# Kernel tuning notes

Measured on AMD Instinct MI355X. Metric: run time of the kernel, lower is better.

The kernel has to match this reference:

```python
import jax, jax.numpy as jnp
import numpy as np

COMMITMENT_COST = 0.25


def setup_inputs() -> dict:
    key = jax.random.key(0)
    k1, k2 = jax.random.split(key)
    ze = jax.random.normal(k1, (16, 256, 32, 32), dtype=jnp.float32)
    codebook = jax.random.normal(k2, (8192, 256), dtype=jnp.float32) * 0.02
    return {"ze": ze, "codebook": codebook}


def reference(ze, codebook):
    # ze: [B, C, H, W] -> [B, H, W, C]
    B, C, H, W = ze.shape
    ze_nhwc = jnp.transpose(ze, (0, 2, 3, 1))
    ze_flat = ze_nhwc.reshape(B * H * W, C)

    # squared L2 distances to every codebook row: [B*H*W, vocab]
    distances = (
        jnp.sum(ze_flat ** 2, axis=1, keepdims=True)
        + jnp.sum(codebook ** 2, axis=1)
        - 2.0 * ze_flat @ codebook.T
    )
    encoding_indices = jnp.argmin(distances, axis=1)  # [B*H*W]
    zq = codebook[encoding_indices].reshape(B, H, W, C)

    sg = jax.lax.stop_gradient
    quantization_loss = jnp.mean((sg(ze_nhwc) - zq) ** 2)
    commitment_loss = jnp.mean((ze_nhwc - sg(zq)) ** 2)
    vq_loss = quantization_loss + COMMITMENT_COST * commitment_loss

    # straight-through estimator (training mode)
    zq = ze_nhwc + sg(zq - ze_nhwc)
    zq = jnp.transpose(zq, (0, 3, 1, 2))  # back to [B, C, H, W]
    return vq_loss, zq, encoding_indices.reshape(B, H * W)
```

## Files before the change

kernel.cpp:

```cpp
#include <hip/hip_runtime.h>
#include <hip/hip_bf16.h>

#define NPIX 16384
#define NVOC 8192
#define CHUNK 32

typedef short short8v __attribute__((ext_vector_type(8)));
typedef float floatx4 __attribute__((ext_vector_type(4)));

#define WS_ZEBF   0u
#define WS_BLIST  0u
#define WS_PART   0u
#define WS_CBBF   8388608u
#define WS_PK     8388608u
#define WS_TAU    8519680u
#define WS_ZEF    12582912u
#define WS_MIN    29360128u
#define WS_BN     37748736u
#define WS_AN     37781504u
#define WS_BCNT   37847040u
#define WS_BMAXU  37847552u
#define WS_QCNT   37847556u
#define WS_QUEUE  37847808u

__device__ __forceinline__ short f2bf(float v) {
  __bf16 h = (__bf16)v;
  return __builtin_bit_cast(short, h);
}

__device__ __forceinline__ float rl(float v, int l) {
  return __uint_as_float(__builtin_amdgcn_readlane(__float_as_uint(v), l));
}

__device__ __forceinline__ unsigned long long packdj(float d, int j) {
  return ((unsigned long long)__float_as_uint(d) << 32) | (unsigned int)j;
}

__device__ __forceinline__ void gll16(const void* g, void* l) {
  __builtin_amdgcn_global_load_lds(
      (const __attribute__((address_space(1))) void*)g,
      (__attribute__((address_space(3))) void*)l, 16, 0, 0);
}

__device__ __forceinline__ float np_pairwise128_sq(const float* x, int stride) {
  float r[8];
#pragma unroll
  for (int j = 0; j < 8; ++j) {
    float v = x[j * stride];
    r[j] = __fmul_rn(v, v);
  }
#pragma unroll
  for (int i = 1; i < 16; ++i) {
#pragma unroll
    for (int j = 0; j < 8; ++j) {
      float v = x[(i * 8 + j) * stride];
      r[j] = __fadd_rn(r[j], __fmul_rn(v, v));
    }
  }
  return __fadd_rn(__fadd_rn(__fadd_rn(r[0], r[1]), __fadd_rn(r[2], r[3])),
                   __fadd_rn(__fadd_rn(r[4], r[5]), __fadd_rn(r[6], r[7])));
}

__global__ __launch_bounds__(256) void k_bnorm(const float* __restrict__ cb,
                                               float* __restrict__ bn,
                                               unsigned* __restrict__ bmaxu) {
  __shared__ float rows[64][257];
  int tid = threadIdx.x;
  int c0 = blockIdx.x * 64;
  for (int r = 0; r < 64; ++r)
    rows[r][tid] = cb[(size_t)(c0 + r) * 256 + tid];
  __syncthreads();
  if (tid < 64) {
    float a = np_pairwise128_sq(&rows[tid][0], 1);
    float b = np_pairwise128_sq(&rows[tid][128], 1);
    float v = __fadd_rn(a, b);
    bn[c0 + tid] = v;
    atomicMax(bmaxu, __float_as_uint(v));
  }
}

__global__ __launch_bounds__(256) void k_cvt_ze(const float* __restrict__ ze,
                                                short* __restrict__ zebff,
                                                float* __restrict__ zef,
                                                float* __restrict__ an) {
  __shared__ float t[64][132];
  int tid = threadIdx.x;
  int p0 = blockIdx.x * 64;
  int b = p0 >> 10, hw0 = p0 & 1023;
  const float* src = ze + (size_t)b * 262144 + hw0;
  float apart = 0.f;
  for (int half = 0; half < 2; ++half) {
    if (half) __syncthreads();
    {
      int hw = tid & 63, cq = tid >> 6;
#pragma unroll
      for (int i = 0; i < 32; ++i) {
        int cl = i * 4 + cq;
        t[hw][cl] = src[(size_t)(half * 128 + cl) * 1024 + hw];
      }
    }
    __syncthreads();
    {
      int r = tid >> 2, cg = tid & 3;
      float* fd = zef + (size_t)(p0 + r) * 256 + half * 128 + cg * 32;
#pragma unroll
      for (int s = 0; s < 8; ++s) {
        float4 v = *reinterpret_cast<const float4*>(&t[r][cg * 32 + s * 4]);
        *reinterpret_cast<float4*>(fd + s * 4) = v;
      }
    }
    {
      int pg_l = tid >> 6, l = tid & 63;
      size_t pg = (size_t)(p0 >> 4) + pg_l;
      int lr = l & 15, lg = l >> 4;
#pragma unroll
      for (int kl = 0; kl < 4; ++kl) {
        int ks = half * 4 + kl;
        short8v v8;
#pragma unroll
        for (int e = 0; e < 8; ++e)
          v8[e] = f2bf(t[pg_l * 16 + lr][kl * 32 + lg * 8 + e]);
        *reinterpret_cast<short8v*>(zebff + (pg * 8 + ks) * 512 + l * 8) = v8;
      }
    }
    if (tid < 64) {
      float a = np_pairwise128_sq(&t[tid][0], 1);
      apart = half ? __fadd_rn(apart, a) : a;
    }
  }
  if (tid < 64) an[p0 + tid] = apart;
}

__global__ __launch_bounds__(256) void k_cvt_cb(const float* __restrict__ cb,
                                                short* __restrict__ cbbft,
                                                unsigned* __restrict__ bmaxu,
                                                int* __restrict__ qcnt) {
  __shared__ short t[64][264];
  int tid = threadIdx.x;
  if (blockIdx.x == 0 && tid == 0) {
    bmaxu[0] = 0u;
    qcnt[0] = 0;
  }
  int j0 = blockIdx.x * 64;
  {
    int col = tid >> 2, q = tid & 3;
    const float* src = cb + (size_t)(j0 + col) * 256 + q * 64;
#pragma unroll
    for (int i = 0; i < 8; ++i) {
      float4 a = *reinterpret_cast<const float4*>(src + i * 8);
      float4 b = *reinterpret_cast<const float4*>(src + i * 8 + 4);
      short8v v;
      v[0] = f2bf(a.x); v[1] = f2bf(a.y); v[2] = f2bf(a.z); v[3] = f2bf(a.w);
      v[4] = f2bf(b.x); v[5] = f2bf(b.y); v[6] = f2bf(b.z); v[7] = f2bf(b.w);
      *reinterpret_cast<short8v*>(&t[col][q * 64 + i * 8]) = v;
    }
  }
  __syncthreads();
  short* dst = cbbft + (size_t)blockIdx.x * 16384;
#pragma unroll
  for (int s = 0; s < 8; ++s) {
    int cid = tid + s * 256;
    int kc = cid >> 6, c2 = cid & 63;
    short8v v = *reinterpret_cast<const short8v*>(&t[c2][kc * 8]);
    *reinterpret_cast<short8v*>(dst + cid * 8) = v;
  }
}

__global__ __launch_bounds__(256, 2) void k_gemm(const short* __restrict__ zebff,
                                                 const short* __restrict__ cbbft,
                                                 const float* __restrict__ bn,
                                                 float* __restrict__ wsmin) {
  __shared__ short lds[32768];
  __shared__ float bnlds[1024];
  int tid = threadIdx.x;
  int lane = tid & 63, w = tid >> 6;
  int g = lane >> 4, r16 = lane & 15;
  int oct = blockIdx.x & 7, chunk = blockIdx.x >> 3;
  int p0 = chunk * 256;
  int ncol0 = oct * 1024;

  short8v pix[4][8];
  {
    const short* base = zebff + ((size_t)(p0 >> 4) + w * 4) * 4096 + lane * 8;
#pragma unroll
    for (int pf = 0; pf < 4; ++pf)
#pragma unroll
      for (int ks = 0; ks < 8; ++ks)
        pix[pf][ks] =
            *reinterpret_cast<const short8v*>(base + pf * 4096 + ks * 512);
  }
  gll16(bn + ncol0 + tid * 4, &bnlds[tid * 4]);

#define STAGE(t, boff)                                                         \
  {                                                                            \
    const short* src_ = cbbft + (size_t)(oct * 16 + (t)) * 16384;              \
    _Pragma("unroll") for (int s = 0; s < 8; ++s) {                            \
      int cid_ = tid + s * 256;                                                \
      gll16(src_ + cid_ * 8, &lds[(boff) + cid_ * 8]);                         \
    }                                                                          \
  }
  STAGE(0, 0)
  asm volatile("s_waitcnt vmcnt(0)" ::: "memory");
  __builtin_amdgcn_s_barrier();

  float* wbase = wsmin + (size_t)(oct * 16) * NPIX + p0 + w * 64 + r16;

  for (int t = 0; t < 16; ++t) {
    int bA = (t & 1) * 16384;
    int bC = bA ^ 16384;
    if (t < 15) STAGE(t + 1, bC)
    float4 bnv[4];
#pragma unroll
    for (int cf = 0; cf < 4; ++cf)
      bnv[cf] =
          *reinterpret_cast<const float4*>(&bnlds[t * 64 + cf * 16 + g * 4]);
    floatx4 acc[4][4];
#pragma unroll
    for (int cf = 0; cf < 4; ++cf)
#pragma unroll
      for (int pf = 0; pf < 4; ++pf) acc[cf][pf] = floatx4{0.f, 0.f, 0.f, 0.f};
    __builtin_amdgcn_s_setprio(1);
#pragma unroll
    for (int ks = 0; ks < 8; ++ks) {
      short8v cfr[4];
#pragma unroll
      for (int cf = 0; cf < 4; ++cf)
        cfr[cf] = *reinterpret_cast<const short8v*>(
            &lds[bA + (((ks * 4 + g) * 64) + cf * 16 + r16) * 8]);
#pragma unroll
      for (int cf = 0; cf < 4; ++cf)
#pragma unroll
        for (int pf = 0; pf < 4; ++pf)
          acc[cf][pf] = __builtin_amdgcn_mfma_f32_16x16x32_bf16(
              cfr[cf], pix[pf][ks], acc[cf][pf], 0, 0, 0);
    }
    __builtin_amdgcn_s_setprio(0);
    float pmin[4];
#pragma unroll
    for (int pf = 0; pf < 4; ++pf) {
      float m_ = 3.4e38f;
#pragma unroll
      for (int cf = 0; cf < 4; ++cf)
#pragma unroll
        for (int rr = 0; rr < 4; ++rr)
          m_ = fminf(m_, __builtin_fmaf(-2.0f, acc[cf][pf][rr], bnv[cf][rr]));
      m_ = fminf(m_, __shfl_xor(m_, 16));
      m_ = fminf(m_, __shfl_xor(m_, 32));
      pmin[pf] = m_;
    }
    if (lane < 16) {
#pragma unroll
      for (int pf = 0; pf < 4; ++pf)
        wbase[(size_t)t * NPIX + pf * 16] = pmin[pf];
    }
    asm volatile("s_waitcnt vmcnt(0)" ::: "memory");
    __builtin_amdgcn_s_barrier();
  }
#undef STAGE
}

__global__ __launch_bounds__(256) void k_tau(const float* __restrict__ wsmin,
                                             const float* __restrict__ an,
                                             const unsigned* __restrict__ bmaxu,
                                             float* __restrict__ tau,
                                             unsigned long long* __restrict__ pk) {
  __shared__ float sm[4][64];
  int tid = threadIdx.x;
  int px = tid & 63, q = tid >> 6;
  int p = blockIdx.x * 64 + px;
  float m0 = 3.4e38f, m1 = 3.4e38f, m2 = 3.4e38f, m3 = 3.4e38f;
#pragma unroll
  for (int i = 0; i < 8; ++i) {
    int c = q * 32 + i * 4;
    m0 = fminf(m0, wsmin[(size_t)c * NPIX + p]);
    m1 = fminf(m1, wsmin[(size_t)(c + 1) * NPIX + p]);
    m2 = fminf(m2, wsmin[(size_t)(c + 2) * NPIX + p]);
    m3 = fminf(m3, wsmin[(size_t)(c + 3) * NPIX + p]);
  }
  sm[q][px] = fminf(fminf(m0, m1), fminf(m2, m3));
  __syncthreads();
  if (tid < 64) {
    float m = fminf(fminf(sm[0][tid], sm[1][tid]), fminf(sm[2][tid], sm[3][tid]));
    float bmaxf = sqrtf(__uint_as_float(bmaxu[0]));
    tau[p] = m + 0.017f * sqrtf(an[p]) * bmaxf + 2e-4f;
    pk[p] = ~0ull;
  }
}

__global__ __launch_bounds__(256) void k_compact(const float* __restrict__ wsmin,
                                                 const float* __restrict__ tau,
                                                 int* __restrict__ bcnt,
                                                 int* __restrict__ blist,
                                                 int* __restrict__ qcnt,
                                                 int* __restrict__ queue) {
  __shared__ int wbase[4];
  __shared__ int running;
  int c = blockIdx.x;
  const float* row = wsmin + (size_t)c * NPIX;
  int* dst = blist + (size_t)c * NPIX;
  int tid = threadIdx.x;
  int lane = tid & 63, wv = tid >> 6;
  if (tid == 0) running = 0;
  __syncthreads();
  for (int base = 0; base < NPIX; base += 256) {
    int p = base + tid;
    bool flag = row[p] <= tau[p];
    unsigned long long mask = __ballot(flag);
    int cnt = __popcll(mask);
    int pre = __popcll(mask & ((1ull << lane) - 1ull));
    if (lane == 0) wbase[wv] = cnt;
    __syncthreads();
    if (tid == 0) {
      int r = running;
#pragma unroll
      for (int w2 = 0; w2 < 4; ++w2) {
        int t = wbase[w2];
        wbase[w2] = r;
        r += t;
      }
      running = r;
    }
    __syncthreads();
    if (flag) dst[wbase[wv] + pre] = p;
    __syncthreads();
  }
  if (tid == 0) {
    int n = running;
    bcnt[c] = n;
    int nch = (n + CHUNK - 1) / CHUNK;
    if (nch > 0) {
      int q0 = atomicAdd(qcnt, nch);
      for (int i = 0; i < nch; ++i) queue[q0 + i] = c | (i << 16);
    }
  }
}

__global__ __launch_bounds__(256) void k_rescore_b(
    const float* __restrict__ zef, const float* __restrict__ cb,
    const float* __restrict__ an, const float* __restrict__ bn,
    const int* __restrict__ bcnt, const int* __restrict__ blist,
    const int* __restrict__ qcnt, const int* __restrict__ queue,
    unsigned long long* __restrict__ pk) {
  __shared__ float cst[256][64];
  int tid = threadIdx.x;
  int lane = tid & 63, wv = tid >> 6;
  int nq = qcnt[0];
  for (int qi = blockIdx.x; qi < nq; qi += 512) {
    int e = queue[qi];
    int c = e & 0xffff;
    int chunk = e >> 16;
    int n = bcnt[c];
    int base = chunk * CHUNK;
    int cnt_here = min(CHUNK, n - base);
    __syncthreads();
    {
      int j = tid >> 2, kq = tid & 3;
      const float* src = cb + (size_t)(c * 64 + j) * 256 + kq * 64;
#pragma unroll
      for (int i = 0; i < 16; ++i) {
        float4 v = *reinterpret_cast<const float4*>(src + i * 4);
        int k = kq * 64 + i * 4;
        cst[k][j] = v.x; cst[k + 1][j] = v.y;
        cst[k + 2][j] = v.z; cst[k + 3][j] = v.w;
      }
    }
    __syncthreads();
    int j_global = c * 64 + lane;
    float bnj = bn[j_global];
    for (int g0 = wv * 4; g0 < cnt_here; g0 += 16) {
      int p[4];
      float4 z[4];
      float ap[4];
#pragma unroll
      for (int gi = 0; gi < 4; ++gi) {
        int idx = base + min(g0 + gi, cnt_here - 1);
        p[gi] = blist[(size_t)c * NPIX + idx];
        z[gi] = *reinterpret_cast<const float4*>(zef + (size_t)p[gi] * 256 +
                                                 lane * 4);
        ap[gi] = an[p[gi]];
      }
      float acc0 = 0.f, acc1 = 0.f, acc2 = 0.f, acc3 = 0.f;
#pragma unroll 8
      for (int k4 = 0; k4 < 64; ++k4) {
#pragma unroll
        for (int kk = 0; kk < 4; ++kk) {
          float cv = cst[k4 * 4 + kk][lane];
          float z0 = (kk == 0) ? z[0].x : (kk == 1) ? z[0].y : (kk == 2) ? z[0].z : z[0].w;
          float z1 = (kk == 0) ? z[1].x : (kk == 1) ? z[1].y : (kk == 2) ? z[1].z : z[1].w;
          float z2 = (kk == 0) ? z[2].x : (kk == 1) ? z[2].y : (kk == 2) ? z[2].z : z[2].w;
          float z3 = (kk == 0) ? z[3].x : (kk == 1) ? z[3].y : (kk == 2) ? z[3].z : z[3].w;
          acc0 = __builtin_fmaf(rl(z0, k4), cv, acc0);
          acc1 = __builtin_fmaf(rl(z1, k4), cv, acc1);
          acc2 = __builtin_fmaf(rl(z2, k4), cv, acc2);
          acc3 = __builtin_fmaf(rl(z3, k4), cv, acc3);
        }
      }
      float dv[4] = {acc0, acc1, acc2, acc3};
#pragma unroll
      for (int gi = 0; gi < 4; ++gi) {
        float d = __fsub_rn(__fadd_rn(ap[gi], bnj), 2.0f * dv[gi]);
        unsigned long long q = packdj(d, j_global);
#pragma unroll
        for (int off = 1; off < 64; off <<= 1) {
          unsigned long long q2 = __shfl_xor(q, off);
          q = q2 < q ? q2 : q;
        }
        if (lane == 0) atomicMin(&pk[p[gi]], q);
      }
    }
  }
}

__global__ __launch_bounds__(256) void k_gather(const float* __restrict__ ze,
                                                const float* __restrict__ cb,
                                                const unsigned long long* __restrict__ pk,
                                                float* __restrict__ out_zq,
                                                float* __restrict__ out_idx,
                                                float* __restrict__ part) {
  __shared__ float qrow[64][257];
  __shared__ int sidx[64];
  int tid = threadIdx.x;
  int p0 = blockIdx.x * 64;
  int b = p0 >> 10, hw0 = p0 & 1023;
  if (tid < 64) {
    int bi = (int)(unsigned int)(pk[p0 + tid] & 0xffffffffull);
    sidx[tid] = bi;
    out_idx[p0 + tid] = (float)bi;
  }
  __syncthreads();
  for (int r = 0; r < 64; ++r)
    qrow[r][tid] = cb[(size_t)sidx[r] * 256 + tid];
  __syncthreads();
  float lsum = 0.f;
  size_t zbase = (size_t)b * 262144 + hw0;
#pragma unroll 4
  for (int i = 0; i < 64; ++i) {
    int px = tid & 63;
    int c = i * 4 + (tid >> 6);
    float qv = qrow[px][c];
    size_t gi = zbase + (size_t)c * 1024 + px;
    float zev = ze[gi];
    out_zq[gi] = __fadd_rn(zev, __fsub_rn(qv, zev));
    float d = zev - qv;
    lsum = __builtin_fmaf(d, d, lsum);
  }
#pragma unroll
  for (int off = 32; off; off >>= 1) lsum += __shfl_xor(lsum, off, 64);
  __shared__ float wsum[4];
  if ((tid & 63) == 0) wsum[tid >> 6] = lsum;
  __syncthreads();
  if (tid == 0) part[blockIdx.x] = (wsum[0] + wsum[1]) + (wsum[2] + wsum[3]);
}

__global__ __launch_bounds__(256) void k_final(const float* __restrict__ part,
                                               float* __restrict__ out0) {
  int tid = threadIdx.x;
  float s = part[tid];
#pragma unroll
  for (int off = 32; off; off >>= 1) s += __shfl_xor(s, off, 64);
  __shared__ float wsum[4];
  if ((tid & 63) == 0) wsum[tid >> 6] = s;
  __syncthreads();
  if (tid == 0)
    out0[0] = 1.25f * ((wsum[0] + wsum[1]) + (wsum[2] + wsum[3])) / 4194304.0f;
}

extern "C" void kernel_launch(void* const* d_in, const int* in_sizes, int n_in,
                              void* d_out, int out_size, void* d_ws, size_t ws_size,
                              hipStream_t stream) {
  const float* ze = (const float*)d_in[0];
  const float* cb = (const float*)d_in[1];
  float* out = (float*)d_out;
  char* ws = (char*)d_ws;
  short* zebff = (short*)(ws + WS_ZEBF);
  short* cbbft = (short*)(ws + WS_CBBF);
  float* zef = (float*)(ws + WS_ZEF);
  float* bn = (float*)(ws + WS_BN);
  float* an = (float*)(ws + WS_AN);
  float* wsmin = (float*)(ws + WS_MIN);
  float* tau = (float*)(ws + WS_TAU);
  int* blist = (int*)(ws + WS_BLIST);
  int* bcnt = (int*)(ws + WS_BCNT);
  unsigned* bmaxu = (unsigned*)(ws + WS_BMAXU);
  int* qcnt = (int*)(ws + WS_QCNT);
  int* queue = (int*)(ws + WS_QUEUE);
  unsigned long long* pk = (unsigned long long*)(ws + WS_PK);
  float* part = (float*)(ws + WS_PART);
  float* out_loss = out;
  float* out_zq = out + 1;
  float* out_idx = out + 1 + 4194304;

  k_cvt_ze<<<256, 256, 0, stream>>>(ze, zebff, zef, an);
  k_cvt_cb<<<128, 256, 0, stream>>>(cb, cbbft, bmaxu, qcnt);
  k_bnorm<<<128, 256, 0, stream>>>(cb, bn, bmaxu);
  k_gemm<<<512, 256, 0, stream>>>(zebff, cbbft, bn, wsmin);
  k_tau<<<256, 256, 0, stream>>>(wsmin, an, bmaxu, tau, pk);
  k_compact<<<128, 256, 0, stream>>>(wsmin, tau, bcnt, blist, qcnt, queue);
  k_rescore_b<<<512, 256, 0, stream>>>(zef, cb, an, bn, bcnt, blist, qcnt,
                                       queue, pk);
  k_gather<<<256, 256, 0, stream>>>(ze, cb, pk, out_zq, out_idx, part);
  k_final<<<1, 256, 0, stream>>>(part, out_loss);
}
```

Baseline: 188.9 us.

## Stage candidate pixels in LDS and use float4 dot products in rescore

The exact fp32 rescore kernel now loads each chunk's 32 candidate pixel vectors into shared memory once. It also stores the codebook block row-major with padding, so each lane reads float4 codebook and pixel values and accumulates 8 pixels per wave. This replaces the per-k readlane broadcasts and the repeated per-wave global loads of pixel vectors, cutting VALU/SALU overhead. The grid shrinks from 512 to 256 blocks because the larger LDS footprint lowers occupancy. Chunks with fewer than 32 pixels now compute padded duplicate rows, which adds redundant work.

```diff
diff --git a/kernel.cpp b/kernel.cpp
--- a/kernel.cpp
+++ b/kernel.cpp
@@ -28,10 +28,6 @@
   return __builtin_bit_cast(short, h);
 }
 
-__device__ __forceinline__ float rl(float v, int l) {
-  return __uint_as_float(__builtin_amdgcn_readlane(__float_as_uint(v), l));
-}
-
 __device__ __forceinline__ unsigned long long packdj(float d, int j) {
   return ((unsigned long long)__float_as_uint(d) << 32) | (unsigned int)j;
 }
@@ -341,11 +337,14 @@
     const int* __restrict__ bcnt, const int* __restrict__ blist,
     const int* __restrict__ qcnt, const int* __restrict__ queue,
     unsigned long long* __restrict__ pk) {
-  __shared__ float cst[256][64];
+  __shared__ float cst[64][257];
+  __shared__ float zl[32][264];
+  __shared__ int pidx[32];
+  __shared__ float apx[32];
   int tid = threadIdx.x;
   int lane = tid & 63, wv = tid >> 6;
   int nq = qcnt[0];
-  for (int qi = blockIdx.x; qi < nq; qi += 512) {
+  for (int qi = blockIdx.x; qi < nq; qi += 256) {
     int e = queue[qi];
     int c = e & 0xffff;
     int chunk = e >> 16;
@@ -354,59 +353,59 @@
     int cnt_here = min(CHUNK, n - base);
     __syncthreads();
     {
-      int j = tid >> 2, kq = tid & 3;
-      const float* src = cb + (size_t)(c * 64 + j) * 256 + kq * 64;
+      int col = tid >> 2, kq = tid & 3;
+      const float* src = cb + (size_t)(c * 64 + col) * 256 + kq * 64;
 #pragma unroll
       for (int i = 0; i < 16; ++i) {
         float4 v = *reinterpret_cast<const float4*>(src + i * 4);
-        int k = kq * 64 + i * 4;
-        cst[k][j] = v.x; cst[k + 1][j] = v.y;
-        cst[k + 2][j] = v.z; cst[k + 3][j] = v.w;
+        *reinterpret_cast<float4*>(&cst[col][kq * 64 + i * 4]) = v;
+      }
+    }
+    {
+      int px = tid >> 3, seg = tid & 7;
+      int idx = base + min(px, cnt_here - 1);
+      int p = blist[(size_t)c * NPIX + idx];
+      const float* src = zef + (size_t)p * 256 + seg * 32;
+#pragma unroll
+      for (int i = 0; i < 8; ++i) {
+        float4 v = *reinterpret_cast<const float4*>(src + i * 4);
+        *reinterpret_cast<float4*>(&zl[px][seg * 32 + i * 4]) = v;
+      }
+      if (seg == 0) {
+        pidx[px] = p;
+        apx[px] = an[p];
       }
     }
     __syncthreads();
     int j_global = c * 64 + lane;
     float bnj = bn[j_global];
-    for (int g0 = wv * 4; g0 < cnt_here; g0 += 16) {
-      int p[4];
-      float4 z[4];
-      float ap[4];
-#pragma unroll
-      for (int gi = 0; gi < 4; ++gi) {
-        int idx = base + min(g0 + gi, cnt_here - 1);
-        p[gi] = blist[(size_t)c * NPIX + idx];
-        z[gi] = *reinterpret_cast<const float4*>(zef + (size_t)p[gi] * 256 +
-                                                 lane * 4);
-        ap[gi] = an[p[gi]];
-      }
-      float acc0 = 0.f, acc1 = 0.f, acc2 = 0.f, acc3 = 0.f;
-#pragma unroll 8
-      for (int k4 = 0; k4 < 64; ++k4) {
-#pragma unroll
-        for (int kk = 0; kk < 4; ++kk) {
-          float cv = cst[k4 * 4 + kk][lane];
-          float z0 = (kk == 0) ? z[0].x : (kk == 1) ? z[0].y : (kk == 2) ? z[0].z : z[0].w;
-          float z1 = (kk == 0) ? z[1].x : (kk == 1) ? z[1].y : (kk == 2) ? z[1].z : z[1].w;
-          float z2 = (kk == 0) ? z[2].x : (kk == 1) ? z[2].y : (kk == 2) ? z[2].z : z[2].w;
-          float z3 = (kk == 0) ? z[3].x : (kk == 1) ? z[3].y : (kk == 2) ? z[3].z : z[3].w;
-          acc0 = __builtin_fmaf(rl(z0, k4), cv, acc0);
-          acc1 = __builtin_fmaf(rl(z1, k4), cv, acc1);
-          acc2 = __builtin_fmaf(rl(z2, k4), cv, acc2);
-          acc3 = __builtin_fmaf(rl(z3, k4), cv, acc3);
-        }
-      }
-      float dv[4] = {acc0, acc1, acc2, acc3};
-#pragma unroll
-      for (int gi = 0; gi < 4; ++gi) {
-        float d = __fsub_rn(__fadd_rn(ap[gi], bnj), 2.0f * dv[gi]);
-        unsigned long long q = packdj(d, j_global);
-#pragma unroll
-        for (int off = 1; off < 64; off <<= 1) {
-          unsigned long long q2 = __shfl_xor(q, off);
-          q = q2 < q ? q2 : q;
-        }
-        if (lane == 0) atomicMin(&pk[p[gi]], q);
-      }
+    float acc[8];
+#pragma unroll
+    for (int i = 0; i < 8; ++i) acc[i] = 0.f;
+#pragma unroll 4
+    for (int k4 = 0; k4 < 64; ++k4) {
+      float4 cv = *reinterpret_cast<const float4*>(&cst[lane][k4 * 4]);
+#pragma unroll
+      for (int i = 0; i < 8; ++i) {
+        float4 zv =
+            *reinterpret_cast<const float4*>(&zl[wv * 8 + i][k4 * 4]);
+        acc[i] = __builtin_fmaf(zv.x, cv.x, acc[i]);
+        acc[i] = __builtin_fmaf(zv.y, cv.y, acc[i]);
+        acc[i] = __builtin_fmaf(zv.z, cv.z, acc[i]);
+        acc[i] = __builtin_fmaf(zv.w, cv.w, acc[i]);
+      }
+    }
+#pragma unroll
+    for (int i = 0; i < 8; ++i) {
+      int px = wv * 8 + i;
+      float d = __fsub_rn(__fadd_rn(apx[px], bnj), 2.0f * acc[i]);
+      unsigned long long q = packdj(d, j_global);
+#pragma unroll
+      for (int off = 1; off < 64; off <<= 1) {
+        unsigned long long q2 = __shfl_xor(q, off);
+        q = q2 < q ? q2 : q;
+      }
+      if (lane == 0) atomicMin(&pk[pidx[px]], q);
     }
   }
 }
@@ -496,7 +495,7 @@
   k_gemm<<<512, 256, 0, stream>>>(zebff, cbbft, bn, wsmin);
   k_tau<<<256, 256, 0, stream>>>(wsmin, an, bmaxu, tau, pk);
   k_compact<<<128, 256, 0, stream>>>(wsmin, tau, bcnt, blist, qcnt, queue);
-  k_rescore_b<<<512, 256, 0, stream>>>(zef, cb, an, bn, bcnt, blist, qcnt,
+  k_rescore_b<<<256, 256, 0, stream>>>(zef, cb, an, bn, bcnt, blist, qcnt,
                                        queue, pk);
   k_gather<<<256, 256, 0, stream>>>(ze, cb, pk, out_zq, out_idx, part);
   k_final<<<1, 256, 0, stream>>>(part, out_loss);
```

After: 192.6 us. About the same (+2.0%).
